# Kernel optimization log

Hardware: AMD Instinct MI355X
Metric: run time of the kernel (lower is better)

## Reference

```python
import jax, jax.numpy as jnp
import numpy as np

B, N, K = 8, 2048, 16          # clouds, points per cloud, knn k
C_IN, C_OUT, H = 64, 128, 64   # channels; H = hidden of pos_nn/attn_nn MLPs


def _init(key, shape, fan_in):
    return jax.random.normal(key, shape, jnp.float32) / np.sqrt(fan_in)


def setup_inputs() -> dict:
    key = jax.random.key(0)
    ks = jax.random.split(key, 20)
    P = B * N
    inp = {
        "x": jax.random.normal(ks[0], (P, C_IN), jnp.float32),
        "pos": jax.random.uniform(ks[1], (P, 3), jnp.float32),
        "batch": jnp.arange(P, dtype=jnp.int64 if jax.config.jax_enable_x64 else jnp.int32) // N,
        # lin_in: in->in, bias
        "Wi": _init(ks[2], (C_IN, C_IN), C_IN), "bi": jnp.zeros((C_IN,), jnp.float32),
        # PointTransformerConv: lin_src/lin_dst/lin are bias-free Linear(in, out)
        "Wsrc": _init(ks[3], (C_IN, C_OUT), C_IN),
        "Wdst": _init(ks[4], (C_IN, C_OUT), C_IN),
        "Wlin": _init(ks[5], (C_IN, C_OUT), C_IN),
        # pos_nn = MLP([3, 64, out], norm=None, plain_last=False): Lin-ReLU-Lin-ReLU
        "Wp1": _init(ks[6], (3, H), 3), "bp1": jnp.zeros((H,), jnp.float32),
        "Wp2": _init(ks[7], (H, C_OUT), H), "bp2": jnp.zeros((C_OUT,), jnp.float32),
        # attn_nn = MLP([out, 64, out], norm=None, plain_last=False)
        "Wa1": _init(ks[8], (C_OUT, H), C_OUT), "ba1": jnp.zeros((H,), jnp.float32),
        "Wa2": _init(ks[9], (H, C_OUT), H), "ba2": jnp.zeros((C_OUT,), jnp.float32),
        # lin_out: out->out, bias
        "Wo": _init(ks[10], (C_OUT, C_OUT), C_OUT), "bo": jnp.zeros((C_OUT,), jnp.float32),
    }
    return inp


def _knn_with_self(pn):
    # pn: [B,N,3] -> neighbor indices [B,N,K+1] = {self} U kNN (excl self),
    # matching knn_graph(loop=False) followed by conv's add_self_loops.
    sq = jnp.sum(pn * pn, -1)                                   # [B,N]
    d2 = sq[:, :, None] + sq[:, None, :] - 2.0 * jnp.einsum("bnd,bmd->bnm", pn, pn)
    d2 = d2 + jnp.eye(N, dtype=pn.dtype) * 1e10                 # exclude self
    _, idx = jax.lax.top_k(-d2, K)                              # [B,N,K]
    self_idx = jnp.broadcast_to(jnp.arange(N)[None, :, None], (B, N, 1))
    return jnp.concatenate([self_idx, idx], axis=-1)            # [B,N,K+1]


def _forward(x, pos, batch, Wi, bi, Wsrc, Wdst, Wlin, Wp1, bp1, Wp2, bp2,
             Wa1, ba1, Wa2, ba2, Wo, bo):
    # batch is structured as B equal-size clouds of N points (see setup_inputs);
    # knn is computed per-cloud, equivalent to knn_graph(pos, k, batch).
    h = jax.nn.relu(x @ Wi + bi).reshape(B, N, C_IN)            # lin_in + relu
    pn = pos.reshape(B, N, 3)
    nbr = _knn_with_self(pn)                                    # [B,N,K+1]

    gather = jax.vmap(lambda t, i: t[i])                        # [N,C],[N,K+1]->[N,K+1,C]

    a_src = h @ Wsrc                                            # [B,N,C_OUT]
    a_dst = h @ Wdst
    v = h @ Wlin

    rel = pn[:, :, None, :] - gather(pn, nbr)                   # pos_i - pos_j [B,N,K+1,3]
    delta = jax.nn.relu(jax.nn.relu(rel @ Wp1 + bp1) @ Wp2 + bp2)   # pos_nn

    alpha = a_dst[:, :, None, :] - gather(a_src, nbr) + delta   # alpha_i - alpha_j + delta
    attn = jax.nn.relu(jax.nn.relu(alpha @ Wa1 + ba1) @ Wa2 + ba2)  # attn_nn
    w = jax.nn.softmax(attn, axis=2)                            # softmax over neighbors

    msg = w * (gather(v, nbr) + delta)                          # [B,N,K+1,C_OUT]
    out = jnp.mean(msg, axis=2)                                 # aggr='mean' (PyG default here)
    out = out.reshape(B * N, C_OUT)
    return jax.nn.relu(out @ Wo + bo)                           # lin_out + relu


def reference(x, pos, batch, Wi, bi, Wsrc, Wdst, Wlin, Wp1, bp1, Wp2, bp2,
              Wa1, ba1, Wa2, ba2, Wo, bo):
    return _forward(x, pos, batch, Wi, bi, Wsrc, Wdst, Wlin, Wp1, bp1, Wp2, bp2,
                    Wa1, ba1, Wa2, ba2, Wo, bo)
```

## Files before the change

kernel.cpp:

```cpp
#include <hip/hip_runtime.h>
#include <hip/hip_fp16.h>

typedef _Float16 h8 __attribute__((ext_vector_type(8)));
typedef _Float16 h4 __attribute__((ext_vector_type(4)));
typedef float fx4 __attribute__((ext_vector_type(4)));

#define NPTS   2048
#define KP1    17
#define PGPT   4
#define EDGES  68
#define ROWS   80
#define MT     5
#define DELTA_OFF 0
#define PH_OFF    20480
#define ATT_OFF   30720
#define SJ_OFF    30720
#define US_OFF    52224
#define NBR_OFF   53248
#define EDGE_SMEM 53568
#define ATT_RB    168

__device__ __forceinline__ int swzA(int row, int bytecol) {
  return (row << 7) + (bytecol ^ ((row & 7) << 4));
}
__device__ __forceinline__ int swzB(int row, int bytecol) {
  return (row << 8) + (bytecol ^ ((row & 7) << 4));
}

#define GH_NB    256
#define WP_NB    32
#define P1_GRID  (GH_NB + WP_NB)

__global__ __launch_bounds__(512) void phase1_kernel(
    const float* __restrict__ x, const float* __restrict__ Wi, const float* __restrict__ bi,
    float* __restrict__ h,
    const float* __restrict__ Wdst, const float* __restrict__ Wsrc,
    const float* __restrict__ Wlin, const float* __restrict__ Wa1,
    float* __restrict__ Wall)
{
  __shared__ __align__(16) char buf[33792];
  const int bid = blockIdx.x;
  const int tid = threadIdx.x;

  if (bid < GH_NB) {
    float* As = (float*)buf;
    float* Ws = (float*)(buf + 64 * 68 * 4);
    long row0 = (long)bid * 64;
    {
      int r = tid >> 3, k8 = (tid & 7) * 8;
      float4 a0 = *(const float4*)(x + (row0 + r) * 64 + k8);
      float4 a1 = *(const float4*)(x + (row0 + r) * 64 + k8 + 4);
      *(float4*)&As[r * 68 + k8] = a0;
      *(float4*)&As[r * 68 + k8 + 4] = a1;
      float4 w0 = *(const float4*)(Wi + r * 64 + k8);
      float4 w1 = *(const float4*)(Wi + r * 64 + k8 + 4);
      *(float4*)&Ws[r * 64 + k8] = w0;
      *(float4*)&Ws[r * 64 + k8 + 4] = w1;
    }
    __syncthreads();
    int tx = tid & 15, ty = tid >> 4;
    float acc[2][4] = {};
#pragma unroll 8
    for (int k = 0; k < 64; ++k) {
      float4 w = *(const float4*)&Ws[k * 64 + tx * 4];
      float a0 = As[(ty * 2 + 0) * 68 + k];
      float a1 = As[(ty * 2 + 1) * 68 + k];
      acc[0][0] += a0 * w.x; acc[0][1] += a0 * w.y; acc[0][2] += a0 * w.z; acc[0][3] += a0 * w.w;
      acc[1][0] += a1 * w.x; acc[1][1] += a1 * w.y; acc[1][2] += a1 * w.z; acc[1][3] += a1 * w.w;
    }
    float b0 = bi[tx * 4 + 0], b1 = bi[tx * 4 + 1], b2 = bi[tx * 4 + 2], b3 = bi[tx * 4 + 3];
#pragma unroll
    for (int i = 0; i < 2; ++i) {
      float4 o;
      o.x = fmaxf(acc[i][0] + b0, 0.f); o.y = fmaxf(acc[i][1] + b1, 0.f);
      o.z = fmaxf(acc[i][2] + b2, 0.f); o.w = fmaxf(acc[i][3] + b3, 0.f);
      *(float4*)(h + (row0 + ty * 2 + i) * 64 + tx * 4) = o;
    }
  } else {
    int gid = (bid - GH_NB) * 512 + tid;
    int q = gid >> 12, r = (gid >> 6) & 63, c = gid & 63;
    float val;
    if (q < 2) {
      const float* W = q ? Wsrc : Wdst;
      float acc = 0.f;
      for (int k = 0; k < 128; ++k) acc += W[r * 128 + k] * Wa1[k * 64 + c];
      val = acc;
    } else {
      val = Wlin[r * 128 + (q - 2) * 64 + c];
    }
    Wall[r * 256 + q * 64 + c] = val;
  }
}

#define KNN_NB 2048
#define UG_NB  1024
#define PK_NB  80
#define K2_GRID (KNN_NB + UG_NB + PK_NB)

__global__ __launch_bounds__(512) void knn_usv_kernel(
    const float* __restrict__ pos, int* __restrict__ nbr, float* __restrict__ rel,
    const float* __restrict__ h, const float* __restrict__ Wall,
    float* __restrict__ usv,
    const float* __restrict__ Wp2, const float* __restrict__ Wa1,
    const float* __restrict__ Wa2, const float* __restrict__ Wo,
    _Float16* __restrict__ p2p, _Float16* __restrict__ a1p, _Float16* __restrict__ a2p,
    _Float16* __restrict__ wop)
{
  __shared__ __align__(16) char buf[33792];
  const int bid = blockIdx.x;
  const int tid = threadIdx.x;

  if (bid < KNN_NB) {
    float* px  = (float*)buf;
    float* py  = (float*)(buf + 8192);
    float* pz  = (float*)(buf + 16384);
    float* sqs = (float*)(buf + 24576);
    int p0 = bid * 8;
    int base = (p0 >> 11) << 11;
    for (int i = tid; i < NPTS; i += 512) {
      float xx = pos[(size_t)(base + i) * 3 + 0];
      float yy = pos[(size_t)(base + i) * 3 + 1];
      float zz = pos[(size_t)(base + i) * 3 + 2];
      px[i] = xx; py[i] = yy; pz[i] = zz;
      sqs[i] = xx * xx + yy * yy + zz * zz;
    }
    __syncthreads();
    int wid = tid >> 6, lane = tid & 63;
    int pl = (p0 & 2047) + wid;
    int gp = base + pl;
    float pix = px[pl], piy = py[pl], piz = pz[pl];

    unsigned key[8];
#pragma unroll
    for (int i = 0; i < 8; ++i) key[i] = 0xFFFFFFFFu;
#pragma unroll
    for (int t = 0; t < 32; ++t) {
      int j = t * 64 + lane;
      float dot = pix * px[j] + piy * py[j] + piz * pz[j];
      float dp = __builtin_fmaf(-2.f, dot, sqs[j]) + 4.0f;
      unsigned kb = (__float_as_uint(dp) & 0xFFFFFFE0u) | (unsigned)t;
      kb = (j == pl) ? 0xFFFFFFFFu : kb;
#pragma unroll
      for (int i = 0; i < 8; ++i) {
        unsigned lo = min(key[i], kb), hi = max(key[i], kb);
        key[i] = lo; kb = hi;
      }
    }

    double pxd = (double)pix, pyd = (double)piy, pzd = (double)piz;
    double sqi64 = pxd * pxd + pyd * pyd + pzd * pzd;
    unsigned long long kk[8];
#pragma unroll
    for (int i = 0; i < 8; ++i) {
      if (key[i] == 0xFFFFFFFFu) { kk[i] = 0xFFFFFFFFFFFFFFFFull; continue; }
      int t = key[i] & 31;
      int j = t * 64 + lane;
      double xj = (double)px[j], yj = (double)py[j], zj = (double)pz[j];
      double sqj = xj * xj + yj * yj + zj * zj;
      double dot = pxd * xj + pyd * yj + pzd * zj;
      double d2 = sqi64 + sqj - 2.0 * dot;
      d2 = d2 > 0.0 ? d2 : 0.0;
      unsigned long long bits = (unsigned long long)__double_as_longlong(d2);
      kk[i] = (bits & ~0x7FFull) | (unsigned long long)j;
    }
#define CE(a, b) { unsigned long long lo_ = kk[a] < kk[b] ? kk[a] : kk[b]; \
                   unsigned long long hi_ = kk[a] < kk[b] ? kk[b] : kk[a]; \
                   kk[a] = lo_; kk[b] = hi_; }
    CE(0,1) CE(2,3) CE(4,5) CE(6,7)
    CE(0,2) CE(1,3) CE(4,6) CE(5,7)
    CE(1,2) CE(5,6) CE(0,4) CE(3,7)
    CE(1,5) CE(2,6)
    CE(1,4) CE(3,6)
    CE(2,4) CE(3,5)
    CE(3,4)
#undef CE

    if (lane == 0) nbr[gp * KP1] = gp;
    if (lane < 3)  rel[(size_t)gp * KP1 * 3 + lane] = 0.f;
    for (int it = 0; it < 16; ++it) {
      unsigned h32 = (unsigned)(kk[0] >> 32);
      unsigned key2 = (h32 & ~63u) | (unsigned)lane;
      unsigned m2 = key2;
#pragma unroll
      for (int off = 32; off > 0; off >>= 1) {
        unsigned o = __shfl_xor(m2, off);
        m2 = o < m2 ? o : m2;
      }
      bool same = ((key2 ^ m2) >> 6) == 0;
      unsigned long long ball = __ballot(same);
      int wl; unsigned jwin;
      if (__popcll(ball) == 1) {
        wl = (int)(m2 & 63u);
        unsigned lo32 = (unsigned)kk[0];
        unsigned wlo = __shfl(lo32, wl);
        jwin = wlo & 2047u;
      } else {
        unsigned long long mk = same ? kk[0] : 0xFFFFFFFFFFFFFFFFull;
#pragma unroll
        for (int off = 32; off > 0; off >>= 1) {
          unsigned long long o = __shfl_xor(mk, off);
          mk = o < mk ? o : mk;
        }
        jwin = (unsigned)(mk & 2047ull);
        wl = (int)(jwin & 63u);
      }
      if (lane == 0) nbr[gp * KP1 + 1 + it] = base + (int)jwin;
      if (lane < 3) {
        const float* ps = lane == 0 ? px : (lane == 1 ? py : pz);
        float pi = lane == 0 ? pix : (lane == 1 ? piy : piz);
        rel[((size_t)gp * KP1 + 1 + it) * 3 + lane] = pi - ps[(int)jwin];
      }
      bool mine = (lane == wl);
#pragma unroll
      for (int i = 0; i < 7; ++i) kk[i] = mine ? kk[i + 1] : kk[i];
      kk[7] = mine ? 0xFFFFFFFFFFFFFFFFull : kk[7];
    }
  } else if (bid < KNN_NB + UG_NB) {
    float* As = (float*)buf;
    float* Ws = (float*)(buf + 64 * 68 * 4);
    int b2 = bid - KNN_NB;
    long row0 = (long)(b2 >> 2) * 64;
    int c0 = (b2 & 3) * 64;
    {
      int r = tid >> 3, k8 = (tid & 7) * 8;
      float4 a0 = *(const float4*)(h + (row0 + r) * 64 + k8);
      float4 a1 = *(const float4*)(h + (row0 + r) * 64 + k8 + 4);
      *(float4*)&As[r * 68 + k8] = a0;
      *(float4*)&As[r * 68 + k8 + 4] = a1;
      float4 w0 = *(const float4*)(Wall + r * 256 + c0 + k8);
      float4 w1 = *(const float4*)(Wall + r * 256 + c0 + k8 + 4);
      *(float4*)&Ws[r * 64 + k8] = w0;
      *(float4*)&Ws[r * 64 + k8 + 4] = w1;
    }
    __syncthreads();
    int tx = tid & 15, ty = tid >> 4;
    float acc[2][4] = {};
#pragma unroll 8
    for (int k = 0; k < 64; ++k) {
      float4 w = *(const float4*)&Ws[k * 64 + tx * 4];
      float a0 = As[(ty * 2 + 0) * 68 + k];
      float a1 = As[(ty * 2 + 1) * 68 + k];
      acc[0][0] += a0 * w.x; acc[0][1] += a0 * w.y; acc[0][2] += a0 * w.z; acc[0][3] += a0 * w.w;
      acc[1][0] += a1 * w.x; acc[1][1] += a1 * w.y; acc[1][2] += a1 * w.z; acc[1][3] += a1 * w.w;
    }
#pragma unroll
    for (int i = 0; i < 2; ++i) {
      float4 o;
      o.x = acc[i][0]; o.y = acc[i][1]; o.z = acc[i][2]; o.w = acc[i][3];
      *(float4*)(usv + (row0 + ty * 2 + i) * 256 + c0 + tx * 4) = o;
    }
  } else {
    int gid = (bid - KNN_NB - UG_NB) * 512 + tid;
    if (gid < 24576) {
      int m = gid >> 13;
      int r = gid & 8191;
      int tl = r >> 9;
      int l  = (r >> 3) & 63;
      int j  = r & 7;
      const float* src; _Float16* dst; int N, kt, nt;
      if (m == 0)      { src = Wp2; dst = p2p; N = 128; kt = tl & 1; nt = tl >> 1; }
      else if (m == 1) { src = Wa1; dst = a1p; N = 64;  kt = tl & 3; nt = tl >> 2; }
      else             { src = Wa2; dst = a2p; N = 128; kt = tl & 1; nt = tl >> 1; }
      int k = kt * 32 + (l >> 4) * 8 + j;
      int n = nt * 16 + (l & 15);
      dst[r] = (_Float16)src[k * N + n];
    } else {
      int r = gid - 24576;
      int tl = r >> 9;
      int l  = (r >> 3) & 63;
      int j  = r & 7;
      int kt = tl & 3, nt = tl >> 2;
      int k = kt * 32 + (l >> 4) * 8 + j;
      int n = nt * 16 + (l & 15);
      wop[r] = (_Float16)Wo[k * 128 + n];
    }
  }
}

__global__ __launch_bounds__(512, 6) void edge_kernel(
    const int* __restrict__ nbr,
    const float* __restrict__ usv,
    const float* __restrict__ rel,
    const float* __restrict__ Wp1, const float* __restrict__ bp1,
    const float* __restrict__ bp2, const float* __restrict__ ba1, const float* __restrict__ ba2,
    const _Float16* __restrict__ Wp2p, const _Float16* __restrict__ Wa1p, const _Float16* __restrict__ Wa2p,
    const _Float16* __restrict__ Wop, const float* __restrict__ bo,
    float* __restrict__ out)
{
  __shared__ __align__(16) char smem[EDGE_SMEM];
  int* nbr_s = (int*)(smem + NBR_OFF);
  float* u_s = (float*)(smem + US_OFF);
  const int tid = threadIdx.x;
  const int lane = tid & 63;
  const int wid = tid >> 6;
  const int bid = blockIdx.x;
  const int pb = ((bid & 7) << 9) | (bid >> 3);
  const int p0 = pb * PGPT;

  if (tid < ROWS) nbr_s[tid] = (tid < EDGES) ? nbr[p0 * KP1 + tid] : p0;
  if (tid < PGPT * 64) u_s[tid] = usv[(size_t)(p0 + (tid >> 6)) * 256 + (tid & 63)];
  __syncthreads();

  const int pp5 = tid >> 7;
  const int c5 = tid & 127;
  float vreg[KP1];
#pragma unroll
  for (int k = 0; k < KP1; ++k) {
    int jv = __builtin_amdgcn_readfirstlane(nbr_s[pp5 * KP1 + k]);
    vreg[k] = usv[(size_t)jv * 256 + 128 + c5];
  }

  {
    float w1x = Wp1[lane], w1y = Wp1[64 + lane], w1z = Wp1[128 + lane], b1 = bp1[lane];
    const float* relb = rel + (size_t)p0 * (KP1 * 3);
    for (int e = wid; e < ROWS; e += 8) {
      int eb = __builtin_amdgcn_readfirstlane(min(e, EDGES - 1));
      int j = __builtin_amdgcn_readfirstlane(nbr_s[eb]);
      float sv = usv[(size_t)j * 256 + 64 + lane];
      *(_Float16*)(smem + SJ_OFF + swzA(e, lane * 2)) = (_Float16)sv;
      float rx = relb[eb * 3 + 0];
      float ry = relb[eb * 3 + 1];
      float rz = relb[eb * 3 + 2];
      float acc = fmaxf(b1 + rx * w1x + ry * w1y + rz * w1z, 0.f);
      *(_Float16*)(smem + PH_OFF + swzA(e, lane * 2)) = (_Float16)acc;
    }
  }
  __syncthreads();

  const int rl = lane & 15;
  const int kl = lane >> 4;

  {
    int nt = wid;
    h8 b0 = *(const h8*)(Wp2p + ((size_t)(nt * 2 + 0) * 64 + lane) * 8);
    h8 b1 = *(const h8*)(Wp2p + ((size_t)(nt * 2 + 1) * 64 + lane) * 8);
    int col = nt * 16 + rl;
    float bias2 = bp2[col];
    for (int mt = 0; mt < MT; ++mt) {
      int arow = mt * 16 + rl;
      h8 a0 = *(const h8*)(smem + PH_OFF + swzA(arow, kl * 16));
      h8 a1 = *(const h8*)(smem + PH_OFF + swzA(arow, 64 + kl * 16));
      fx4 acc = {0.f, 0.f, 0.f, 0.f};
      acc = __builtin_amdgcn_mfma_f32_16x16x32_f16(a0, b0, acc, 0, 0, 0);
      acc = __builtin_amdgcn_mfma_f32_16x16x32_f16(a1, b1, acc, 0, 0, 0);
#pragma unroll
      for (int jj = 0; jj < 4; ++jj) {
        int orow = mt * 16 + kl * 4 + jj;
        float val = fmaxf(acc[jj] + bias2, 0.f);
        *(_Float16*)(smem + DELTA_OFF + swzB(orow, col * 2)) = (_Float16)val;
      }
    }
  }
  __syncthreads();

  {
    int nt = wid & 3;
    h8 b[4];
#pragma unroll
    for (int kt = 0; kt < 4; ++kt)
      b[kt] = *(const h8*)(Wa1p + ((size_t)(nt * 4 + kt) * 64 + lane) * 8);
    int hcol = nt * 16 + rl;
    float b1v = ba1[hcol];
    for (int mt = (wid >> 2); mt < MT; mt += 2) {
      int arow = mt * 16 + rl;
      fx4 acc = {0.f, 0.f, 0.f, 0.f};
#pragma unroll
      for (int kt = 0; kt < 4; ++kt) {
        h8 a = *(const h8*)(smem + DELTA_OFF + swzB(arow, kt * 64 + kl * 16));
        acc = __builtin_amdgcn_mfma_f32_16x16x32_f16(a, b[kt], acc, 0, 0, 0);
      }
#pragma unroll
      for (int jj = 0; jj < 4; ++jj) {
        int orow = mt * 16 + kl * 4 + jj;
        int oc = min(orow, EDGES - 1);
        int p = (oc * 241) >> 12;
        float uu = u_s[p * 64 + hcol];
        float ss = (float)*(const _Float16*)(smem + SJ_OFF + swzA(orow, hcol * 2));
        float val = fmaxf(acc[jj] + uu - ss + b1v, 0.f);
        *(_Float16*)(smem + PH_OFF + swzA(orow, hcol * 2)) = (_Float16)val;
      }
    }
  }
  __syncthreads();

  {
    int nt = wid;
    h8 b0 = *(const h8*)(Wa2p + ((size_t)(nt * 2 + 0) * 64 + lane) * 8);
    h8 b1 = *(const h8*)(Wa2p + ((size_t)(nt * 2 + 1) * 64 + lane) * 8);
    int col = nt * 16 + rl;
    float b2v = ba2[col];
    char* cbase = smem + ATT_OFF + col * ATT_RB;
    for (int mt = 0; mt < MT; ++mt) {
      int arow = mt * 16 + rl;
      h8 a0 = *(const h8*)(smem + PH_OFF + swzA(arow, kl * 16));
      h8 a1 = *(const h8*)(smem + PH_OFF + swzA(arow, 64 + kl * 16));
      fx4 acc = {0.f, 0.f, 0.f, 0.f};
      acc = __builtin_amdgcn_mfma_f32_16x16x32_f16(a0, b0, acc, 0, 0, 0);
      acc = __builtin_amdgcn_mfma_f32_16x16x32_f16(a1, b1, acc, 0, 0, 0);
#pragma unroll
      for (int jj = 0; jj < 4; ++jj) {
        int orow = mt * 16 + kl * 4 + jj;
        if (orow < EDGES) {
          int pp = (orow * 241) >> 12;
          float val = fmaxf(acc[jj] + b2v, 0.f);
          *(_Float16*)(cbase + (orow + 3 * pp) * 2) = (_Float16)val;
        }
      }
    }
  }
  __syncthreads();

  h8 bw[4];
#pragma unroll
  for (int kt = 0; kt < 4; ++kt)
    bw[kt] = *(const h8*)(Wop + ((size_t)(wid * 4 + kt) * 64 + lane) * 8);

  {
    int r0 = pp5 * KP1;
    const char* abase = smem + ATT_OFF + c5 * ATT_RB + pp5 * 40;
    h4 t0 = *(const h4*)(abase + 0);
    h4 t1 = *(const h4*)(abase + 8);
    h4 t2 = *(const h4*)(abase + 16);
    h4 t3 = *(const h4*)(abase + 24);
    float att[KP1];
#pragma unroll
    for (int q = 0; q < 4; ++q) {
      att[0 + q]  = (float)t0[q];
      att[4 + q]  = (float)t1[q];
      att[8 + q]  = (float)t2[q];
      att[12 + q] = (float)t3[q];
    }
    att[16] = (float)*(const _Float16*)(abase + 32);
    float m8[8];
#pragma unroll
    for (int k = 0; k < 8; ++k) m8[k] = fmaxf(att[k], att[k + 8]);
    float m4a = fmaxf(m8[0], m8[1]), m4b = fmaxf(m8[2], m8[3]);
    float m4c = fmaxf(m8[4], m8[5]), m4d = fmaxf(m8[6], m8[7]);
    float m = fmaxf(fmaxf(fmaxf(m4a, m4b), fmaxf(m4c, m4d)), att[16]);
    float den = 0.f;
#pragma unroll
    for (int k = 0; k < KP1; ++k) { att[k] = __expf(att[k] - m); den += att[k]; }
    float inv = 1.f / (den * 17.f);
    float acc = 0.f;
#pragma unroll
    for (int k = 0; k < KP1; ++k) {
      float dd = (float)*(const _Float16*)(smem + DELTA_OFF + swzB(r0 + k, c5 * 2));
      acc += att[k] * (vreg[k] + dd);
    }
    *(_Float16*)(smem + PH_OFF + swzB(pp5, c5 * 2)) = (_Float16)(acc * inv);
  }
  __syncthreads();

  {
    fx4 acc = {0.f, 0.f, 0.f, 0.f};
#pragma unroll
    for (int kt = 0; kt < 4; ++kt) {
      h8 a = *(const h8*)(smem + PH_OFF + swzB(rl, kt * 64 + kl * 16));
      acc = __builtin_amdgcn_mfma_f32_16x16x32_f16(a, bw[kt], acc, 0, 0, 0);
    }
    if (kl == 0) {
      int col = wid * 16 + rl;
      float bov = bo[col];
#pragma unroll
      for (int jj = 0; jj < 4; ++jj)
        out[(size_t)(p0 + jj) * 128 + col] = fmaxf(acc[jj] + bov, 0.f);
    }
  }
}

extern "C" void kernel_launch(void* const* d_in, const int* in_sizes, int n_in,
                              void* d_out, int out_size, void* d_ws, size_t ws_size,
                              hipStream_t stream) {
  const float* x    = (const float*)d_in[0];
  const float* pos  = (const float*)d_in[1];
  const float* Wi   = (const float*)d_in[3];
  const float* bi   = (const float*)d_in[4];
  const float* Wsrc = (const float*)d_in[5];
  const float* Wdst = (const float*)d_in[6];
  const float* Wlin = (const float*)d_in[7];
  const float* Wp1  = (const float*)d_in[8];
  const float* bp1  = (const float*)d_in[9];
  const float* Wp2  = (const float*)d_in[10];
  const float* bp2  = (const float*)d_in[11];
  const float* Wa1  = (const float*)d_in[12];
  const float* ba1  = (const float*)d_in[13];
  const float* Wa2  = (const float*)d_in[14];
  const float* ba2  = (const float*)d_in[15];
  const float* Wo   = (const float*)d_in[16];
  const float* bo   = (const float*)d_in[17];
  float* out = (float*)d_out;

  char* ws = (char*)d_ws;
  float* h    = (float*)(ws + 0);
  float* usv  = (float*)(ws + 4194304);
  float* Wall = (float*)(ws + 20971520);
  float* rel  = (float*)(ws + 21037056);
  int*   nbr  = (int*)  (ws + 29360128);
  _Float16* p2p = (_Float16*)(ws + 30474240);
  _Float16* a1p = (_Float16*)(ws + 30490624);
  _Float16* a2p = (_Float16*)(ws + 30507008);
  _Float16* wop = (_Float16*)(ws + 30523392);

  phase1_kernel<<<P1_GRID, 512, 0, stream>>>(x, Wi, bi, h, Wdst, Wsrc, Wlin, Wa1, Wall);
  knn_usv_kernel<<<K2_GRID, 512, 0, stream>>>(pos, nbr, rel, h, Wall, usv,
                                              Wp2, Wa1, Wa2, Wo, p2p, a1p, a2p, wop);
  edge_kernel<<<4096, 512, 0, stream>>>(nbr, usv, rel, Wp1, bp1, bp2, ba1, ba2,
                                        p2p, a1p, a2p, wop, bo, out);
}
```

Measured before the change: 138.2 us.

## Process two query points per wavefront in kNN with packed float4 positions

Each kNN wavefront now handles two query points, so each candidate position loaded from LDS is reused for two distance computations, and the number of kNN blocks is halved. Positions and squared norms are packed into a single float4 in shared memory so one vector LDS load replaces four scalar loads. A wave-wide __any test skips the 8-deep insertion network when no lane's candidate beats its current 8th-best key. In exchange each thread holds more registers for two key arrays, the refinement and selection stages for the two queries run one after the other, and there are fewer blocks to spread across the GPU.

```diff
diff --git a/kernel.cpp b/kernel.cpp
--- a/kernel.cpp
+++ b/kernel.cpp
@@ -92,7 +92,7 @@
   }
 }
 
-#define KNN_NB 2048
+#define KNN_NB 1024
 #define UG_NB  1024
 #define PK_NB  80
 #define K2_GRID (KNN_NB + UG_NB + PK_NB)
@@ -111,109 +111,134 @@
   const int tid = threadIdx.x;
 
   if (bid < KNN_NB) {
-    float* px  = (float*)buf;
-    float* py  = (float*)(buf + 8192);
-    float* pz  = (float*)(buf + 16384);
-    float* sqs = (float*)(buf + 24576);
-    int p0 = bid * 8;
+    float4* pc = (float4*)buf;
+    int p0 = bid * 16;
     int base = (p0 >> 11) << 11;
     for (int i = tid; i < NPTS; i += 512) {
       float xx = pos[(size_t)(base + i) * 3 + 0];
       float yy = pos[(size_t)(base + i) * 3 + 1];
       float zz = pos[(size_t)(base + i) * 3 + 2];
-      px[i] = xx; py[i] = yy; pz[i] = zz;
-      sqs[i] = xx * xx + yy * yy + zz * zz;
+      float4 v; v.x = xx; v.y = yy; v.z = zz; v.w = xx * xx + yy * yy + zz * zz;
+      pc[i] = v;
     }
     __syncthreads();
     int wid = tid >> 6, lane = tid & 63;
-    int pl = (p0 & 2047) + wid;
-    int gp = base + pl;
-    float pix = px[pl], piy = py[pl], piz = pz[pl];
-
-    unsigned key[8];
-#pragma unroll
-    for (int i = 0; i < 8; ++i) key[i] = 0xFFFFFFFFu;
+    int pl0 = (p0 & 2047) + wid * 2;
+    int pl1 = pl0 + 1;
+    float4 qp0 = pc[pl0];
+    float4 qp1 = pc[pl1];
+
+    unsigned key0[8], key1[8];
+#pragma unroll
+    for (int i = 0; i < 8; ++i) { key0[i] = 0xFFFFFFFFu; key1[i] = 0xFFFFFFFFu; }
 #pragma unroll
     for (int t = 0; t < 32; ++t) {
       int j = t * 64 + lane;
-      float dot = pix * px[j] + piy * py[j] + piz * pz[j];
-      float dp = __builtin_fmaf(-2.f, dot, sqs[j]) + 4.0f;
-      unsigned kb = (__float_as_uint(dp) & 0xFFFFFFE0u) | (unsigned)t;
-      kb = (j == pl) ? 0xFFFFFFFFu : kb;
+      float4 c = pc[j];
+      {
+        float dot = qp0.x * c.x + qp0.y * c.y + qp0.z * c.z;
+        float dp = __builtin_fmaf(-2.f, dot, c.w) + 4.0f;
+        unsigned kb = (__float_as_uint(dp) & 0xFFFFFFE0u) | (unsigned)t;
+        kb = (j == pl0) ? 0xFFFFFFFFu : kb;
+        if (__any(kb < key0[7])) {
+#pragma unroll
+          for (int i = 0; i < 8; ++i) {
+            unsigned lo = min(key0[i], kb), hi = max(key0[i], kb);
+            key0[i] = lo; kb = hi;
+          }
+        }
+      }
+      {
+        float dot = qp1.x * c.x + qp1.y * c.y + qp1.z * c.z;
+        float dp = __builtin_fmaf(-2.f, dot, c.w) + 4.0f;
+        unsigned kb = (__float_as_uint(dp) & 0xFFFFFFE0u) | (unsigned)t;
+        kb = (j == pl1) ? 0xFFFFFFFFu : kb;
+        if (__any(kb < key1[7])) {
+#pragma unroll
+          for (int i = 0; i < 8; ++i) {
+            unsigned lo = min(key1[i], kb), hi = max(key1[i], kb);
+            key1[i] = lo; kb = hi;
+          }
+        }
+      }
+    }
+
+#pragma unroll 1
+    for (int q = 0; q < 2; ++q) {
+      int pl = q ? pl1 : pl0;
+      int gp = base + pl;
+      float4 qp = q ? qp1 : qp0;
+
+      double pxd = (double)qp.x, pyd = (double)qp.y, pzd = (double)qp.z;
+      double sqi64 = pxd * pxd + pyd * pyd + pzd * pzd;
+      unsigned long long kk[8];
 #pragma unroll
       for (int i = 0; i < 8; ++i) {
-        unsigned lo = min(key[i], kb), hi = max(key[i], kb);
-        key[i] = lo; kb = hi;
-      }
-    }
-
-    double pxd = (double)pix, pyd = (double)piy, pzd = (double)piz;
-    double sqi64 = pxd * pxd + pyd * pyd + pzd * pzd;
-    unsigned long long kk[8];
-#pragma unroll
-    for (int i = 0; i < 8; ++i) {
-      if (key[i] == 0xFFFFFFFFu) { kk[i] = 0xFFFFFFFFFFFFFFFFull; continue; }
-      int t = key[i] & 31;
-      int j = t * 64 + lane;
-      double xj = (double)px[j], yj = (double)py[j], zj = (double)pz[j];
-      double sqj = xj * xj + yj * yj + zj * zj;
-      double dot = pxd * xj + pyd * yj + pzd * zj;
-      double d2 = sqi64 + sqj - 2.0 * dot;
-      d2 = d2 > 0.0 ? d2 : 0.0;
-      unsigned long long bits = (unsigned long long)__double_as_longlong(d2);
-      kk[i] = (bits & ~0x7FFull) | (unsigned long long)j;
-    }
+        unsigned ky = q ? key1[i] : key0[i];
+        if (ky == 0xFFFFFFFFu) { kk[i] = 0xFFFFFFFFFFFFFFFFull; continue; }
+        int t = ky & 31;
+        int j = t * 64 + lane;
+        float4 c = pc[j];
+        double xj = (double)c.x, yj = (double)c.y, zj = (double)c.z;
+        double sqj = xj * xj + yj * yj + zj * zj;
+        double dot = pxd * xj + pyd * yj + pzd * zj;
+        double d2 = sqi64 + sqj - 2.0 * dot;
+        d2 = d2 > 0.0 ? d2 : 0.0;
+        unsigned long long bits = (unsigned long long)__double_as_longlong(d2);
+        kk[i] = (bits & ~0x7FFull) | (unsigned long long)j;
+      }
 #define CE(a, b) { unsigned long long lo_ = kk[a] < kk[b] ? kk[a] : kk[b]; \
                    unsigned long long hi_ = kk[a] < kk[b] ? kk[b] : kk[a]; \
                    kk[a] = lo_; kk[b] = hi_; }
-    CE(0,1) CE(2,3) CE(4,5) CE(6,7)
-    CE(0,2) CE(1,3) CE(4,6) CE(5,7)
-    CE(1,2) CE(5,6) CE(0,4) CE(3,7)
-    CE(1,5) CE(2,6)
-    CE(1,4) CE(3,6)
-    CE(2,4) CE(3,5)
-    CE(3,4)
+      CE(0,1) CE(2,3) CE(4,5) CE(6,7)
+      CE(0,2) CE(1,3) CE(4,6) CE(5,7)
+      CE(1,2) CE(5,6) CE(0,4) CE(3,7)
+      CE(1,5) CE(2,6)
+      CE(1,4) CE(3,6)
+      CE(2,4) CE(3,5)
+      CE(3,4)
 #undef CE
 
-    if (lane == 0) nbr[gp * KP1] = gp;
-    if (lane < 3)  rel[(size_t)gp * KP1 * 3 + lane] = 0.f;
-    for (int it = 0; it < 16; ++it) {
-      unsigned h32 = (unsigned)(kk[0] >> 32);
-      unsigned key2 = (h32 & ~63u) | (unsigned)lane;
-      unsigned m2 = key2;
-#pragma unroll
-      for (int off = 32; off > 0; off >>= 1) {
-        unsigned o = __shfl_xor(m2, off);
-        m2 = o < m2 ? o : m2;
-      }
-      bool same = ((key2 ^ m2) >> 6) == 0;
-      unsigned long long ball = __ballot(same);
-      int wl; unsigned jwin;
-      if (__popcll(ball) == 1) {
-        wl = (int)(m2 & 63u);
-        unsigned lo32 = (unsigned)kk[0];
-        unsigned wlo = __shfl(lo32, wl);
-        jwin = wlo & 2047u;
-      } else {
-        unsigned long long mk = same ? kk[0] : 0xFFFFFFFFFFFFFFFFull;
+      if (lane == 0) nbr[gp * KP1] = gp;
+      if (lane < 3)  rel[(size_t)gp * KP1 * 3 + lane] = 0.f;
+      for (int it = 0; it < 16; ++it) {
+        unsigned h32 = (unsigned)(kk[0] >> 32);
+        unsigned key2 = (h32 & ~63u) | (unsigned)lane;
+        unsigned m2 = key2;
 #pragma unroll
         for (int off = 32; off > 0; off >>= 1) {
-          unsigned long long o = __shfl_xor(mk, off);
-          mk = o < mk ? o : mk;
+          unsigned o = __shfl_xor(m2, off);
+          m2 = o < m2 ? o : m2;
         }
-        jwin = (unsigned)(mk & 2047ull);
-        wl = (int)(jwin & 63u);
-      }
-      if (lane == 0) nbr[gp * KP1 + 1 + it] = base + (int)jwin;
-      if (lane < 3) {
-        const float* ps = lane == 0 ? px : (lane == 1 ? py : pz);
-        float pi = lane == 0 ? pix : (lane == 1 ? piy : piz);
-        rel[((size_t)gp * KP1 + 1 + it) * 3 + lane] = pi - ps[(int)jwin];
-      }
-      bool mine = (lane == wl);
-#pragma unroll
-      for (int i = 0; i < 7; ++i) kk[i] = mine ? kk[i + 1] : kk[i];
-      kk[7] = mine ? 0xFFFFFFFFFFFFFFFFull : kk[7];
+        bool same = ((key2 ^ m2) >> 6) == 0;
+        unsigned long long ball = __ballot(same);
+        int wl; unsigned jwin;
+        if (__popcll(ball) == 1) {
+          wl = (int)(m2 & 63u);
+          unsigned lo32 = (unsigned)kk[0];
+          unsigned wlo = __shfl(lo32, wl);
+          jwin = wlo & 2047u;
+        } else {
+          unsigned long long mk = same ? kk[0] : 0xFFFFFFFFFFFFFFFFull;
+#pragma unroll
+          for (int off = 32; off > 0; off >>= 1) {
+            unsigned long long o = __shfl_xor(mk, off);
+            mk = o < mk ? o : mk;
+          }
+          jwin = (unsigned)(mk & 2047ull);
+          wl = (int)(jwin & 63u);
+        }
+        if (lane == 0) nbr[gp * KP1 + 1 + it] = base + (int)jwin;
+        if (lane < 3) {
+          float pi = lane == 0 ? qp.x : (lane == 1 ? qp.y : qp.z);
+          float pj = ((const float*)&pc[(int)jwin])[lane];
+          rel[((size_t)gp * KP1 + 1 + it) * 3 + lane] = pi - pj;
+        }
+        bool mine = (lane == wl);
+#pragma unroll
+        for (int i = 0; i < 7; ++i) kk[i] = mine ? kk[i + 1] : kk[i];
+        kk[7] = mine ? 0xFFFFFFFFFFFFFFFFull : kk[7];
+      }
     }
   } else if (bid < KNN_NB + UG_NB) {
     float* As = (float*)buf;
```

After: 140.2 us. No clear change (+1.4%).

## Process three points per edge-kernel block to pad fewer MFMA rows

Applied to the files above, without the earlier changes.

Changes the edge kernel to handle 3 points (51 edges padded to 64 rows, 4 M-tiles) per block instead of 4 points (68 edges padded to 80 rows, 5 M-tiles). This cuts padded MFMA work and shrinks LDS use, which allows a higher occupancy launch bound. The cost is more blocks, bounds checks for the ragged tail, per-edge index math for rel and nbr loads, and one idle wave group in the softmax/aggregate stage.

```diff
diff --git a/kernel.cpp b/kernel.cpp
--- a/kernel.cpp
+++ b/kernel.cpp
@@ -6,19 +6,21 @@
 typedef float fx4 __attribute__((ext_vector_type(4)));
 
 #define NPTS   2048
+#define POINTS 16384
 #define KP1    17
-#define PGPT   4
-#define EDGES  68
-#define ROWS   80
-#define MT     5
+#define PGPT   3
+#define EDGES  51
+#define ROWS   64
+#define MT     4
+#define EDGE_NB 5462
 #define DELTA_OFF 0
-#define PH_OFF    20480
-#define ATT_OFF   30720
-#define SJ_OFF    30720
-#define US_OFF    52224
-#define NBR_OFF   53248
-#define EDGE_SMEM 53568
-#define ATT_RB    168
+#define PH_OFF    16384
+#define SJ_OFF    24576
+#define ATT_OFF   24576
+#define US_OFF    39936
+#define NBR_OFF   40704
+#define EDGE_SMEM 40960
+#define ATT_RB    120
 
 __device__ __forceinline__ int swzA(int row, int bytecol) {
   return (row << 7) + (bytecol ^ ((row & 7) << 4));
@@ -277,7 +279,7 @@
   }
 }
 
-__global__ __launch_bounds__(512, 6) void edge_kernel(
+__global__ __launch_bounds__(512, 8) void edge_kernel(
     const int* __restrict__ nbr,
     const float* __restrict__ usv,
     const float* __restrict__ rel,
@@ -294,33 +296,48 @@
   const int lane = tid & 63;
   const int wid = tid >> 6;
   const int bid = blockIdx.x;
-  const int pb = ((bid & 7) << 9) | (bid >> 3);
+  const int k8 = bid & 7, i8 = bid >> 3;
+  const int q8 = EDGE_NB >> 3, r8 = EDGE_NB & 7;
+  const int pb = (k8 < r8 ? k8 * (q8 + 1) : r8 * (q8 + 1) + (k8 - r8) * q8) + i8;
   const int p0 = pb * PGPT;
 
-  if (tid < ROWS) nbr_s[tid] = (tid < EDGES) ? nbr[p0 * KP1 + tid] : p0;
-  if (tid < PGPT * 64) u_s[tid] = usv[(size_t)(p0 + (tid >> 6)) * 256 + (tid & 63)];
+  if (tid < ROWS) {
+    int ec = min(tid, EDGES - 1);
+    int pp = (ec * 241) >> 12;
+    int ep = min(p0 + pp, POINTS - 1);
+    nbr_s[tid] = nbr[ep * KP1 + (ec - pp * KP1)];
+  }
+  if (tid < PGPT * 64) {
+    int ep = min(p0 + (tid >> 6), POINTS - 1);
+    u_s[tid] = usv[(size_t)ep * 256 + (tid & 63)];
+  }
   __syncthreads();
 
   const int pp5 = tid >> 7;
   const int c5 = tid & 127;
+  const bool act5 = pp5 < PGPT;
   float vreg[KP1];
-#pragma unroll
-  for (int k = 0; k < KP1; ++k) {
-    int jv = __builtin_amdgcn_readfirstlane(nbr_s[pp5 * KP1 + k]);
-    vreg[k] = usv[(size_t)jv * 256 + 128 + c5];
+  if (act5) {
+#pragma unroll
+    for (int k = 0; k < KP1; ++k) {
+      int jv = __builtin_amdgcn_readfirstlane(nbr_s[pp5 * KP1 + k]);
+      vreg[k] = usv[(size_t)jv * 256 + 128 + c5];
+    }
   }
 
   {
     float w1x = Wp1[lane], w1y = Wp1[64 + lane], w1z = Wp1[128 + lane], b1 = bp1[lane];
-    const float* relb = rel + (size_t)p0 * (KP1 * 3);
     for (int e = wid; e < ROWS; e += 8) {
       int eb = __builtin_amdgcn_readfirstlane(min(e, EDGES - 1));
+      int pp = (eb * 241) >> 12;
+      int ep = min(p0 + pp, POINTS - 1);
+      int ei = ep * KP1 + (eb - pp * KP1);
       int j = __builtin_amdgcn_readfirstlane(nbr_s[eb]);
       float sv = usv[(size_t)j * 256 + 64 + lane];
       *(_Float16*)(smem + SJ_OFF + swzA(e, lane * 2)) = (_Float16)sv;
-      float rx = relb[eb * 3 + 0];
-      float ry = relb[eb * 3 + 1];
-      float rz = relb[eb * 3 + 2];
+      float rx = rel[(size_t)ei * 3 + 0];
+      float ry = rel[(size_t)ei * 3 + 1];
+      float rz = rel[(size_t)ei * 3 + 2];
       float acc = fmaxf(b1 + rx * w1x + ry * w1y + rz * w1z, 0.f);
       *(_Float16*)(smem + PH_OFF + swzA(e, lane * 2)) = (_Float16)acc;
     }
@@ -415,7 +432,7 @@
   for (int kt = 0; kt < 4; ++kt)
     bw[kt] = *(const h8*)(Wop + ((size_t)(wid * 4 + kt) * 64 + lane) * 8);
 
-  {
+  if (act5) {
     int r0 = pp5 * KP1;
     const char* abase = smem + ATT_OFF + c5 * ATT_RB + pp5 * 40;
     h4 t0 = *(const h4*)(abase + 0);
@@ -462,8 +479,9 @@
       int col = wid * 16 + rl;
       float bov = bo[col];
 #pragma unroll
-      for (int jj = 0; jj < 4; ++jj)
-        out[(size_t)(p0 + jj) * 128 + col] = fmaxf(acc[jj] + bov, 0.f);
+      for (int jj = 0; jj < 3; ++jj)
+        if (p0 + jj < POINTS)
+          out[(size_t)(p0 + jj) * 128 + col] = fmaxf(acc[jj] + bov, 0.f);
     }
   }
 }
@@ -504,6 +522,6 @@
   phase1_kernel<<<P1_GRID, 512, 0, stream>>>(x, Wi, bi, h, Wdst, Wsrc, Wlin, Wa1, Wall);
   knn_usv_kernel<<<K2_GRID, 512, 0, stream>>>(pos, nbr, rel, h, Wall, usv,
                                               Wp2, Wa1, Wa2, Wo, p2p, a1p, a2p, wop);
-  edge_kernel<<<4096, 512, 0, stream>>>(nbr, usv, rel, Wp1, bp1, bp2, ba1, ba2,
-                                        p2p, a1p, a2p, wop, bo, out);
+  edge_kernel<<<EDGE_NB, 512, 0, stream>>>(nbr, usv, rel, Wp1, bp1, bp2, ba1, ba2,
+                                           p2p, a1p, a2p, wop, bo, out);
 }
```

Result: slower. 151.1 us (+9.3%).
